# Performance work log

Hardware: AMD Instinct MI355X
Metric: run time of the kernel (lower is better)

Reference implementation:

```python
import jax, jax.numpy as jnp
import numpy as np

D = 4096      # square linear: in_features == out_features (required by the module's math)
RANK = 8
ALPHA = 16.0
SCALE = ALPHA / RANK


def setup_inputs() -> dict:
    key = jax.random.key(0)
    kx, kw, kb, ka = jax.random.split(key, 4)
    x = jax.random.normal(kx, (8, 2048, D), dtype=jnp.float32)
    # torch nn.Linear weight is (out_features, in_features); forward is x @ W.T + b
    W = jax.random.normal(kw, (D, D), dtype=jnp.float32) * 0.02
    b = jax.random.normal(kb, (D,), dtype=jnp.float32) * 0.02
    # module init: lora_a ~ N(0, 0.02), lora_b = zeros
    lora_a = jax.random.normal(ka, (RANK, D), dtype=jnp.float32) * 0.02  # (rank, output_d)
    lora_b = jnp.zeros((D, RANK), dtype=jnp.float32)                     # (input_d, rank)
    return {"x": x, "W": W, "b": b, "lora_a": lora_a, "lora_b": lora_b}


def reference(x, W, b, lora_a, lora_b):
    # base linear: y = x @ W.T + b
    base = jnp.einsum("bsd,od->bso", x, W) + b
    # LoRA path: x @ (lora_b @ lora_a) * alpha / rank
    # (computed factored as (x @ lora_b) @ lora_a -- same math, avoids the DxD materialization)
    lora = jnp.einsum("bsr,rd->bsd", jnp.einsum("bsd,dr->bsr", x, lora_b), lora_a)
    return base + lora * SCALE
```

## Files before the change

kernel.cpp:

```cpp
#include <hip/hip_runtime.h>


#define GM 16384
#define GN 4096
#define GK 4096
#define SCALE_C 2.0f

typedef __attribute__((ext_vector_type(8))) short short8;
typedef __attribute__((ext_vector_type(8))) unsigned short ushort8;
typedef __attribute__((ext_vector_type(4))) float float4_;

typedef const __attribute__((address_space(1))) void gvoid;
typedef __attribute__((address_space(3))) void svoid;

__device__ __forceinline__ void gload16(const void* g, void* s) {
    __builtin_amdgcn_global_load_lds((gvoid*)g, (svoid*)s, 16, 0, 0);
}

__device__ __forceinline__ unsigned short f2bf(float f) {
    union { float f; unsigned u; } v; v.f = f;
    unsigned r = v.u + 0x7FFFu + ((v.u >> 16) & 1u);
    return (unsigned short)(r >> 16);
}

__global__ void cast_x_ts(const float* __restrict__ x, const float* __restrict__ lora_b,
                          unsigned short* __restrict__ Xb, float* __restrict__ ts) {
    const int m = blockIdx.x;
    const int tid = threadIdx.x;
    const size_t rowoff = (size_t)m * GK;
    const int d0 = tid * 16;

    const float4_* xp = (const float4_*)(x + rowoff + d0);
    float4_ xv[4];
#pragma unroll
    for (int u = 0; u < 4; ++u) xv[u] = xp[u];

    ushort8 h0, h1;
#pragma unroll
    for (int u = 0; u < 8; ++u) h0[u] = f2bf(xv[u / 4][u % 4]);
#pragma unroll
    for (int u = 0; u < 8; ++u) h1[u] = f2bf(xv[2 + u / 4][u % 4]);
    *(ushort8*)(Xb + rowoff + d0) = h0;
    *(ushort8*)(Xb + rowoff + d0 + 8) = h1;

    float t[8] = {0.f,0.f,0.f,0.f,0.f,0.f,0.f,0.f};
#pragma unroll
    for (int u = 0; u < 16; ++u) {
        float xf = xv[u / 4][u % 4];
        const float4_* lb = (const float4_*)(lora_b + (size_t)(d0 + u) * 8);
        float4_ b0 = lb[0], b1 = lb[1];
#pragma unroll
        for (int r = 0; r < 4; ++r) { t[r] += xf * b0[r]; t[4 + r] += xf * b1[r]; }
    }
#pragma unroll
    for (int off = 32; off >= 1; off >>= 1) {
#pragma unroll
        for (int r = 0; r < 8; ++r) t[r] += __shfl_down(t[r], off, 64);
    }
    __shared__ float red[4][8];
    const int lane = tid & 63, wave = tid >> 6;
    if (lane == 0) {
#pragma unroll
        for (int r = 0; r < 8; ++r) red[wave][r] = t[r];
    }
    __syncthreads();
    if (tid < 8) {
        float s = red[0][tid] + red[1][tid] + red[2][tid] + red[3][tid];
        ts[(size_t)m * 8 + tid] = s * SCALE_C;
    }
}

__global__ void cast_w(const float* __restrict__ W, unsigned short* __restrict__ Wb) {
    const size_t i = ((size_t)blockIdx.x * 256 + threadIdx.x) * 8;
    const float4_* p = (const float4_*)(W + i);
    float4_ a = p[0], b = p[1];
    ushort8 h;
#pragma unroll
    for (int r = 0; r < 4; ++r) { h[r] = f2bf(a[r]); h[4 + r] = f2bf(b[r]); }
    *(ushort8*)(Wb + i) = h;
}

__global__ void gemm_bt(const unsigned short* __restrict__ A, const unsigned short* __restrict__ B,
                        const float* __restrict__ bias, const float* __restrict__ ts,
                        const float* __restrict__ la, float* __restrict__ out) {
    __shared__ unsigned short lA[128 * 64];
    __shared__ unsigned short lB[128 * 64];

    const int tid = threadIdx.x;
    const int lane = tid & 63;
    const int wave = tid >> 6;
    const int wr = wave >> 1, wc = wave & 1;
    const int m0 = blockIdx.y * 128;
    const int n0 = blockIdx.x * 128;

    float4_ acc[4][4] = {};

    const int r8 = tid >> 3;
    const int c16 = (tid & 7) << 4;

    const char* gA = (const char*)(A + (size_t)m0 * GK);
    const char* gB = (const char*)(B + (size_t)n0 * GK);
    char* sA = (char*)lA;
    char* sB = (char*)lB;

    for (int kt = 0; kt < GK; kt += 64) {
#pragma unroll
        for (int g = 0; g < 4; ++g) {
            const int row = g * 32 + r8;
            const int gc = c16 ^ ((row & 7) << 4);
            gload16(gA + (size_t)row * (GK * 2) + (size_t)kt * 2 + gc, sA + row * 128 + c16);
            gload16(gB + (size_t)row * (GK * 2) + (size_t)kt * 2 + gc, sB + row * 128 + c16);
        }
        __syncthreads();

#pragma unroll
        for (int kk = 0; kk < 64; kk += 32) {
            const int colb = (kk + (lane >> 4) * 8) * 2;
            short8 av[4], bv[4];
#pragma unroll
            for (int i = 0; i < 4; ++i) {
                const int row = wr * 64 + i * 16 + (lane & 15);
                av[i] = *(const short8*)(sA + row * 128 + (colb ^ ((row & 7) << 4)));
            }
#pragma unroll
            for (int j = 0; j < 4; ++j) {
                const int row = wc * 64 + j * 16 + (lane & 15);
                bv[j] = *(const short8*)(sB + row * 128 + (colb ^ ((row & 7) << 4)));
            }
#pragma unroll
            for (int i = 0; i < 4; ++i)
#pragma unroll
                for (int j = 0; j < 4; ++j)
                    acc[i][j] = __builtin_amdgcn_mfma_f32_16x16x32_bf16(av[i], bv[j], acc[i][j], 0, 0, 0);
        }
        __syncthreads();
    }

    const int lrow = lane & 15, kgrp = lane >> 4;
    float areg[4][8];
    float bj[4];
    int ocol[4];
#pragma unroll
    for (int j = 0; j < 4; ++j) {
        const int o = n0 + wc * 64 + j * 16 + lrow;
        ocol[j] = o;
        bj[j] = bias[o];
#pragma unroll
        for (int r = 0; r < 8; ++r) areg[j][r] = la[(size_t)r * GN + o];
    }
#pragma unroll
    for (int i = 0; i < 4; ++i) {
#pragma unroll
        for (int reg = 0; reg < 4; ++reg) {
            const int m = m0 + wr * 64 + i * 16 + kgrp * 4 + reg;
            const float4_* tp = (const float4_*)(ts + (size_t)m * 8);
            const float4_ t0 = tp[0], t1 = tp[1];
            float* orow = out + (size_t)m * GN;
#pragma unroll
            for (int j = 0; j < 4; ++j) {
                const float lor = t0[0]*areg[j][0] + t0[1]*areg[j][1] + t0[2]*areg[j][2] + t0[3]*areg[j][3]
                                + t1[0]*areg[j][4] + t1[1]*areg[j][5] + t1[2]*areg[j][6] + t1[3]*areg[j][7];
                orow[ocol[j]] = acc[i][j][reg] + bj[j] + lor;
            }
        }
    }
}

extern "C" void kernel_launch(void* const* d_in, const int* in_sizes, int n_in,
                              void* d_out, int out_size, void* d_ws, size_t ws_size,
                              hipStream_t stream) {
    const float* x      = (const float*)d_in[0];
    const float* W      = (const float*)d_in[1];
    const float* b      = (const float*)d_in[2];
    const float* lora_a = (const float*)d_in[3];
    const float* lora_b = (const float*)d_in[4];
    float* out = (float*)d_out;

    char* ws = (char*)d_ws;
    unsigned short* Xb = (unsigned short*)ws;
    unsigned short* Wb = (unsigned short*)(ws + (size_t)134217728);
    float*          ts = (float*)(ws + (size_t)134217728 + 33554432);

    cast_x_ts<<<GM, 256, 0, stream>>>(x, lora_b, Xb, ts);
    cast_w<<<GN * GK / (256 * 8), 256, 0, stream>>>(W, Wb);
    gemm_bt<<<dim3(GN / 128, GM / 128), 256, 0, stream>>>(Xb, Wb, b, ts, lora_a, out);
}
```

Baseline: 1.219 ms.

## Replace GEMM with 256x256-tile 8-wave double-buffered pipelined kernel

Rewrites the main bf16 GEMM to use 256x256 output tiles with 512 threads (8 waves), a double-buffered 128KB LDS ping-pong, and staged global->LDS loads interleaved with four MFMA phases per K-tile. It also raises MFMA priority around the compute phases and remaps workgroup IDs for L2 locality. The aim is to hide global load latency behind the matrix ops and raise arithmetic intensity per LDS byte. The cost is heavier register pressure from 8x4 accumulators and many more barriers per tile.

```diff
diff --git a/kernel.cpp b/kernel.cpp
--- a/kernel.cpp
+++ b/kernel.cpp
@@ -4,6 +4,7 @@
 #define GM 16384
 #define GN 4096
 #define GK 4096
+#define NT (GK / 64)
 #define SCALE_C 2.0f
 
 typedef __attribute__((ext_vector_type(8))) short short8;
@@ -80,87 +81,138 @@
     *(ushort8*)(Wb + i) = h;
 }
 
-__global__ void gemm_bt(const unsigned short* __restrict__ A, const unsigned short* __restrict__ B,
-                        const float* __restrict__ bias, const float* __restrict__ ts,
-                        const float* __restrict__ la, float* __restrict__ out) {
-    __shared__ unsigned short lA[128 * 64];
-    __shared__ unsigned short lB[128 * 64];
+
+#define BARRIER __builtin_amdgcn_s_barrier()
+#define PRIO1 __builtin_amdgcn_s_setprio(1)
+#define PRIO0 __builtin_amdgcn_s_setprio(0)
+
+#define MM8(AH, BH, FO, JO)                                                    \
+    _Pragma("unroll") for (int kk = 0; kk < 2; ++kk)                           \
+    _Pragma("unroll") for (int f = 0; f < 4; ++f)                              \
+    _Pragma("unroll") for (int j = 0; j < 2; ++j)                              \
+        acc[(FO) + f][(JO) + j] = __builtin_amdgcn_mfma_f32_16x16x32_bf16(     \
+            AH[f][kk], BH[j][kk], acc[(FO) + f][(JO) + j], 0, 0, 0)
+
+#define STAGE(G, LB, KT, H)                                                    \
+    do {                                                                       \
+        _Pragma("unroll") for (int l = 0; l < 2; ++l)                          \
+            gload16((G) + (size_t)((H) * 128 + wave * 16 + l * 8 + ln8) * (GK * 2) \
+                        + (size_t)(KT) * 128 + sgc,                            \
+                    ldsc + (LB) + (H) * 16384 + (wave * 128 + l * 64 + lane) * 16); \
+    } while (0)
+
+#define KTILE_BODY(T, SA, SB, VMC)                                             \
+    do {                                                                       \
+        const int b_ = (T) & 1;                                                \
+        const int Ab_ = b_ * 65536, Bb_ = Ab_ + 32768;                         \
+        const int An_ = (1 - b_) * 65536;                                      \
+        short8 al[4][2], ah[4][2], bl[2][2], bh[2][2];                         \
+                                                                      \
+        _Pragma("unroll") for (int f = 0; f < 4; ++f)                          \
+        _Pragma("unroll") for (int kk = 0; kk < 2; ++kk)                       \
+            al[f][kk] = *(const short8*)(ldsc + Ab_ + (wm * 128 + f * 16 + l15) * 128 + cofs[kk]); \
+        _Pragma("unroll") for (int j = 0; j < 2; ++j)                          \
+        _Pragma("unroll") for (int kk = 0; kk < 2; ++kk)                       \
+            bl[j][kk] = *(const short8*)(ldsc + Bb_ + (wn * 64 + j * 16 + l15) * 128 + cofs[kk]); \
+        if (SA) STAGE(gA, An_, (T) + 1, 0);                                    \
+        BARRIER;                                                               \
+        PRIO1; MM8(al, bl, 0, 0); PRIO0;                                       \
+        BARRIER;                                                               \
+                                                                      \
+        _Pragma("unroll") for (int j = 0; j < 2; ++j)                          \
+        _Pragma("unroll") for (int kk = 0; kk < 2; ++kk)                       \
+            bh[j][kk] = *(const short8*)(ldsc + Bb_ + (wn * 64 + (2 + j) * 16 + l15) * 128 + cofs[kk]); \
+        if (SA) STAGE(gA, An_, (T) + 1, 1);                                    \
+        BARRIER;                                                               \
+        PRIO1; MM8(al, bh, 0, 2); PRIO0;                                       \
+        BARRIER;                                                               \
+                                                                      \
+        _Pragma("unroll") for (int f = 0; f < 4; ++f)                          \
+        _Pragma("unroll") for (int kk = 0; kk < 2; ++kk)                       \
+            ah[f][kk] = *(const short8*)(ldsc + Ab_ + (wm * 128 + (4 + f) * 16 + l15) * 128 + cofs[kk]); \
+        if (SB) STAGE(gB, Bb_, (T) + 2, 0);                                    \
+        BARRIER;                                                               \
+        PRIO1; MM8(ah, bh, 4, 2); PRIO0;                                       \
+        BARRIER;                                                               \
+                                                                      \
+        if (SB) STAGE(gB, Bb_, (T) + 2, 1);                                    \
+        if ((VMC) == 4) asm volatile("s_waitcnt vmcnt(4)" ::: "memory");       \
+        if ((VMC) == 0) asm volatile("s_waitcnt vmcnt(0)" ::: "memory");       \
+        BARRIER;                                                               \
+        PRIO1; MM8(ah, bl, 4, 0); PRIO0;                                       \
+        BARRIER;                                                               \
+    } while (0)
+
+__global__ __launch_bounds__(512, 2) void gemm8p(
+        const unsigned short* __restrict__ A, const unsigned short* __restrict__ B,
+        const float* __restrict__ bias, const float* __restrict__ ts,
+        const float* __restrict__ la, float* __restrict__ out) {
+    __shared__ char ldsbuf[131072];
+    char* ldsc = ldsbuf;
 
     const int tid = threadIdx.x;
     const int lane = tid & 63;
     const int wave = tid >> 6;
-    const int wr = wave >> 1, wc = wave & 1;
-    const int m0 = blockIdx.y * 128;
-    const int n0 = blockIdx.x * 128;
-
-    float4_ acc[4][4] = {};
-
-    const int r8 = tid >> 3;
-    const int c16 = (tid & 7) << 4;
-
-    const char* gA = (const char*)(A + (size_t)m0 * GK);
-    const char* gB = (const char*)(B + (size_t)n0 * GK);
-    char* sA = (char*)lA;
-    char* sB = (char*)lB;
-
-    for (int kt = 0; kt < GK; kt += 64) {
-#pragma unroll
-        for (int g = 0; g < 4; ++g) {
-            const int row = g * 32 + r8;
-            const int gc = c16 ^ ((row & 7) << 4);
-            gload16(gA + (size_t)row * (GK * 2) + (size_t)kt * 2 + gc, sA + row * 128 + c16);
-            gload16(gB + (size_t)row * (GK * 2) + (size_t)kt * 2 + gc, sB + row * 128 + c16);
-        }
-        __syncthreads();
-
-#pragma unroll
-        for (int kk = 0; kk < 64; kk += 32) {
-            const int colb = (kk + (lane >> 4) * 8) * 2;
-            short8 av[4], bv[4];
-#pragma unroll
-            for (int i = 0; i < 4; ++i) {
-                const int row = wr * 64 + i * 16 + (lane & 15);
-                av[i] = *(const short8*)(sA + row * 128 + (colb ^ ((row & 7) << 4)));
-            }
-#pragma unroll
-            for (int j = 0; j < 4; ++j) {
-                const int row = wc * 64 + j * 16 + (lane & 15);
-                bv[j] = *(const short8*)(sB + row * 128 + (colb ^ ((row & 7) << 4)));
-            }
-#pragma unroll
-            for (int i = 0; i < 4; ++i)
-#pragma unroll
-                for (int j = 0; j < 4; ++j)
-                    acc[i][j] = __builtin_amdgcn_mfma_f32_16x16x32_bf16(av[i], bv[j], acc[i][j], 0, 0, 0);
-        }
-        __syncthreads();
-    }
-
-    const int lrow = lane & 15, kgrp = lane >> 4;
-    float areg[4][8];
-    float bj[4];
+    const int wm = wave >> 2;
+    const int wn = wave & 3;
+    const int l15 = lane & 15;
+    const int ln8 = lane >> 3;
+
+    int wg = (int)blockIdx.x;
+    wg = (wg & 7) * 128 + (wg >> 3);
+    const int tm = wg >> 4, tn = wg & 15;
+    const size_t m0 = (size_t)tm * 256, n0 = (size_t)tn * 256;
+
+    const char* gA = (const char*)(A + m0 * GK);
+    const char* gB = (const char*)(B + n0 * GK);
+
+    const int sgc = ((lane & 7) << 4) ^ (ln8 << 4);
+    int cofs[2];
+#pragma unroll
+    for (int kk = 0; kk < 2; ++kk)
+        cofs[kk] = (kk * 64 + ((lane >> 4) << 4)) ^ ((lane & 7) << 4);
+
+    float4_ acc[8][4] = {};
+
+    STAGE(gA, 0, 0, 0);
+    STAGE(gA, 0, 0, 1);
+    STAGE(gB, 32768, 0, 0);
+    STAGE(gB, 32768, 0, 1);
+    STAGE(gB, 65536 + 32768, 1, 0);
+    STAGE(gB, 65536 + 32768, 1, 1);
+    asm volatile("s_waitcnt vmcnt(4)" ::: "memory");
+    BARRIER;
+
+    for (int t = 0; t < NT - 2; ++t) {
+        KTILE_BODY(t, 1, 1, 4);
+    }
+    KTILE_BODY(NT - 2, 1, 0, 0);
+    KTILE_BODY(NT - 1, 0, 0, -1);
+
+    const int kg = lane >> 4;
+    float bj[4], areg[4][8];
     int ocol[4];
 #pragma unroll
     for (int j = 0; j < 4; ++j) {
-        const int o = n0 + wc * 64 + j * 16 + lrow;
+        const int o = (int)n0 + wn * 64 + j * 16 + l15;
         ocol[j] = o;
         bj[j] = bias[o];
 #pragma unroll
         for (int r = 0; r < 8; ++r) areg[j][r] = la[(size_t)r * GN + o];
     }
 #pragma unroll
-    for (int i = 0; i < 4; ++i) {
+    for (int f = 0; f < 8; ++f) {
 #pragma unroll
         for (int reg = 0; reg < 4; ++reg) {
-            const int m = m0 + wr * 64 + i * 16 + kgrp * 4 + reg;
-            const float4_* tp = (const float4_*)(ts + (size_t)m * 8);
+            const size_t m = m0 + wm * 128 + f * 16 + kg * 4 + reg;
+            const float4_* tp = (const float4_*)(ts + m * 8);
             const float4_ t0 = tp[0], t1 = tp[1];
-            float* orow = out + (size_t)m * GN;
+            float* orow = out + m * GN;
 #pragma unroll
             for (int j = 0; j < 4; ++j) {
                 const float lor = t0[0]*areg[j][0] + t0[1]*areg[j][1] + t0[2]*areg[j][2] + t0[3]*areg[j][3]
                                 + t1[0]*areg[j][4] + t1[1]*areg[j][5] + t1[2]*areg[j][6] + t1[3]*areg[j][7];
-                orow[ocol[j]] = acc[i][j][reg] + bj[j] + lor;
+                orow[ocol[j]] = acc[f][j][reg] + bj[j] + lor;
             }
         }
     }
@@ -183,5 +235,5 @@
 
     cast_x_ts<<<GM, 256, 0, stream>>>(x, lora_b, Xb, ts);
     cast_w<<<GN * GK / (256 * 8), 256, 0, stream>>>(W, Wb);
-    gemm_bt<<<dim3(GN / 128, GM / 128), 256, 0, stream>>>(Xb, Wb, b, ts, lora_a, out);
-}
+    gemm8p<<<(GM / 256) * (GN / 256), 512, 0, stream>>>(Xb, Wb, b, ts, lora_a, out);
+}
```

New measurement: 1.178 ms. 3.4% less time.
